# Performance work log

Measured on AMD Instinct MI355X. Metric: run time of the kernel, lower is better.

Reference implementation:

```python
import jax, jax.numpy as jnp
import numpy as np

B, IN, C, M = 256, 512, 4, 6
S1, S2 = 255, 63          # neurons per layer excluding the prepended bias unit
K = 2 ** M                # contexts per neuron
P = 1e-3                  # pred_clipping
LMIN = float(np.log(P / (1.0 - P)))
LMAX = -LMIN
LR = 1e-3                 # constant learning rate
WCLIP = 5.0               # weight_clipping
BASE_BIAS = 0.0           # fixed base bias logit (original draws uniform in [LMIN, LMAX])


def setup_inputs() -> dict:
    key = jax.random.key(0)
    ks = jax.random.split(key, 10)
    x = jax.random.uniform(ks[0], (B, IN), dtype=jnp.float32)
    target = jax.random.randint(ks[1], (B,), 0, C, dtype=jnp.int32)
    cmaps1 = jax.random.normal(ks[2], (C, S1, M, IN), dtype=jnp.float32)
    w1 = jax.random.uniform(ks[3], (C, S1, K, IN), dtype=jnp.float32) * (2.0 / IN)
    bias1 = jax.random.uniform(ks[4], (1, 1, C), dtype=jnp.float32, minval=LMIN, maxval=LMAX)
    cmaps2 = jax.random.normal(ks[5], (C, S2, M, IN), dtype=jnp.float32)
    w2 = jax.random.uniform(ks[6], (C, S2, K, S1 + 1), dtype=jnp.float32) * (2.0 / (S1 + 1))
    bias2 = jax.random.uniform(ks[7], (1, 1, C), dtype=jnp.float32, minval=LMIN, maxval=LMAX)
    cmaps3 = jax.random.normal(ks[8], (C, 1, M, IN), dtype=jnp.float32)
    w3 = jax.random.uniform(ks[9], (C, 1, K, S2 + 1), dtype=jnp.float32) * (2.0 / (S2 + 1))
    return {"x": x, "target": target, "cmaps1": cmaps1, "w1": w1, "bias1": bias1,
            "cmaps2": cmaps2, "w2": w2, "bias2": bias2, "cmaps3": cmaps3, "w3": w3}


def _layer(logit3, context, tgt, cmaps, weights, bias):
    # logit3: (B, I, Cin) with Cin in {1, C}; context: (B, IN); tgt: (B, C) one-hot
    # cmaps: (C, S, M, IN); weights: (C, S, K, I)
    Cn, S = weights.shape[0], weights.shape[1]
    Bn = context.shape[0]
    # context halfspace gating -> per-(class, neuron, sample) context index
    dist = jnp.einsum('csmk,bk->csmb', cmaps, context)          # (C,S,M,B)
    conv = (2 ** jnp.arange(M, dtype=jnp.int32)).reshape(1, 1, M, 1)
    idx = jnp.sum((dist > 0.0).astype(jnp.int32) * conv, axis=2)  # (C,S,B)
    ci = jnp.arange(Cn)[:, None, None]
    si = jnp.arange(S)[None, :, None]
    sel = weights[ci, si, idx]                                  # gather: (C,S,B,I)
    lg = jnp.broadcast_to(logit3, (Bn, logit3.shape[1], Cn))    # (B,I,C)
    out = jnp.clip(jnp.einsum('csbi,bic->csb', sel, lg), LMIN, LMAX)
    out_t = jnp.transpose(out, (2, 1, 0))                       # (B,S,C)
    # online gradient-style update scattered back into the weight table
    diff = jax.nn.sigmoid(out_t) - tgt[:, None, :]              # (B,S,C)
    upd = LR * diff[..., None] * jnp.transpose(lg, (0, 2, 1))[:, None, :, :]  # (B,S,C,I)
    new_w = weights.at[ci, si, idx].set(
        jnp.clip(sel - jnp.transpose(upd, (2, 1, 0, 3)), -WCLIP, WCLIP))
    if bias is not None:
        out_t = jnp.concatenate([jnp.broadcast_to(bias, (Bn, 1, Cn)), out_t], axis=1)
    return out_t, new_w


def reference(x, target, cmaps1, w1, bias1, cmaps2, w2, bias2, cmaps3, w3):
    tgt = jax.nn.one_hot(target, C, dtype=x.dtype)              # (B,C)
    xb = jnp.clip(x, P, 1.0 - P)
    l0 = jnp.log(xb / (1.0 - xb)).at[:, 0].set(BASE_BIAS)       # base predictions in logit space
    out1, nw1 = _layer(l0[:, :, None], x, tgt, cmaps1, w1, bias1)  # (B,256,C)
    out2, nw2 = _layer(out1, x, tgt, cmaps2, w2, bias2)            # (B,64,C)
    out3, nw3 = _layer(out2, x, tgt, cmaps3, w3, None)             # (B,1,C)
    logits = out3[:, 0, :]                                         # (B,C)
    return (logits, nw1, nw2, nw3)
```

## Files before the change

### kernel.cpp

```cpp
#include <hip/hip_runtime.h>
#include <math.h>

#define B_   256
#define IN_  512
#define C_   4
#define M_   6
#define K_   64
#define S1_  255
#define S2_  63

#define NBLK1 (C_ * S1_)
#define NBLK2 (C_ * S2_)
#define NBLK3 (C_)
#define NBLK_ALL (NBLK1 + NBLK2 + NBLK3)

#define LMIN_ (-6.906754778648554f)
#define LMAX_ ( 6.906754778648554f)
#define LR_   0.001f
#define WCLIP_ 5.0f

typedef float v4f __attribute__((ext_vector_type(4)));

__device__ __forceinline__ float clampf(float v, float lo, float hi) {
    return fminf(fmaxf(v, lo), hi);
}

__global__ __launch_bounds__(256) void prep_kernel(const float* __restrict__ x,
                                                   const float* __restrict__ bias1,
                                                   const float* __restrict__ bias2,
                                                   float* __restrict__ xT,
                                                   float* __restrict__ l0,
                                                   float* __restrict__ l0T,
                                                   float* __restrict__ out1T,
                                                   float* __restrict__ out1RM,
                                                   float* __restrict__ out2T,
                                                   float* __restrict__ out2RM) {
    __shared__ float tx_[32][33];
    __shared__ float tl_[32][33];
    const int i0 = (blockIdx.x & 15) * 32;
    const int b0 = (blockIdx.x >> 4) * 32;
    const int tx = threadIdx.x & 31;
    const int ty = threadIdx.x >> 5;
#pragma unroll
    for (int r = 0; r < 4; ++r) {
        int bb = b0 + ty + 8 * r;
        int ii = i0 + tx;
        float xv = x[(size_t)bb * IN_ + ii];
        float xc = clampf(xv, 0.001f, 0.999f);
        float lv = (ii == 0) ? 0.0f : logf(xc / (1.0f - xc));
        l0[(size_t)bb * IN_ + ii] = lv;
        tx_[ty + 8 * r][tx] = xv;
        tl_[ty + 8 * r][tx] = lv;
    }
    __syncthreads();
#pragma unroll
    for (int r = 0; r < 4; ++r) {
        int ii = i0 + ty + 8 * r;
        int bb = b0 + tx;
        xT[(size_t)ii * B_ + bb]  = tx_[tx][ty + 8 * r];
        l0T[(size_t)ii * B_ + bb] = tl_[tx][ty + 8 * r];
    }
    int gid = blockIdx.x * 256 + threadIdx.x;
    if (gid < C_ * B_) {
        int c = gid >> 8, b = gid & 255;
        float b1 = bias1[c], b2 = bias2[c];
        out1T[((size_t)c * (S1_ + 1)) * B_ + b] = b1;
        out1RM[((size_t)c * B_ + b) * (S1_ + 1)] = b1;
        out2T[((size_t)c * (S2_ + 1)) * B_ + b] = b2;
        out2RM[((size_t)c * B_ + b) * (S2_ + 1)] = b2;
    }
}

__global__ __launch_bounds__(256) void route_kernel(
    const float* __restrict__ xT,
    const float* __restrict__ cmaps1,
    const float* __restrict__ cmaps2,
    const float* __restrict__ cmaps3,
    int* __restrict__ idx_buf)
{
    __shared__ float sacc[3][2][M_][B_];
    const int wv   = __builtin_amdgcn_readfirstlane(threadIdx.x >> 6);
    const int lane = threadIdx.x & 63;
    const int t0   = blockIdx.x * 2;

    const float* cmp[2];
#pragma unroll
    for (int u = 0; u < 2; ++u) {
        int bid = t0 + u;
        if (bid < NBLK1)              cmp[u] = cmaps1 + (size_t)bid * M_ * IN_;
        else if (bid < NBLK1 + NBLK2) cmp[u] = cmaps2 + (size_t)(bid - NBLK1) * M_ * IN_;
        else                          cmp[u] = cmaps3 + (size_t)(bid - NBLK1 - NBLK2) * M_ * IN_;
    }

    float acc[2][4][M_];
#pragma unroll
    for (int u = 0; u < 2; ++u)
#pragma unroll
        for (int jb = 0; jb < 4; ++jb)
#pragma unroll
            for (int m = 0; m < M_; ++m) acc[u][jb][m] = 0.0f;

    const int kw = wv * 128;
    for (int k0 = kw; k0 < kw + 128; k0 += 8) {
        float xv[8][4];
#pragma unroll
        for (int j = 0; j < 8; ++j)
#pragma unroll
            for (int jb = 0; jb < 4; ++jb)
                xv[j][jb] = xT[(size_t)(k0 + j) * B_ + 64 * jb + lane];
#pragma unroll
        for (int j = 0; j < 8; ++j)
#pragma unroll
            for (int u = 0; u < 2; ++u)
#pragma unroll
                for (int m = 0; m < M_; ++m) {
                    float cv = cmp[u][(size_t)m * IN_ + k0 + j];
#pragma unroll
                    for (int jb = 0; jb < 4; ++jb)
                        acc[u][jb][m] = fmaf(cv, xv[j][jb], acc[u][jb][m]);
                }
    }

    if (wv > 0) {
#pragma unroll
        for (int u = 0; u < 2; ++u)
#pragma unroll
            for (int jb = 0; jb < 4; ++jb)
#pragma unroll
                for (int m = 0; m < M_; ++m)
                    sacc[wv - 1][u][m][64 * jb + lane] = acc[u][jb][m];
    }
    __syncthreads();
    if (wv == 0) {
#pragma unroll
        for (int u = 0; u < 2; ++u)
#pragma unroll
            for (int jb = 0; jb < 4; ++jb) {
                int b = 64 * jb + lane;
                int myidx = 0;
#pragma unroll
                for (int m = 0; m < M_; ++m) {
                    float t = acc[u][jb][m] + sacc[0][u][m][b] + sacc[1][u][m][b] + sacc[2][u][m][b];
                    myidx |= (t > 0.0f) ? (1 << m) : 0;
                }
                idx_buf[(size_t)(t0 + u) * B_ + b] = myidx;
            }
    }
}

template<int DIN>
__device__ __forceinline__ void dotfin_body(
    int tile,
    const float* __restrict__ lgT, long lgT_sc,
    const float* __restrict__ w,
    const int* __restrict__ idx_buf,
    const int* __restrict__ target,
    float* __restrict__ onextT,
    float* __restrict__ onextRM,
    int* __restrict__ win_g,
    float* __restrict__ dw_g,
    int S,
    float* wl, float* part_s, float* diff_s, int* win_s)
{
    constexpr int HALF = DIN / 2;
    constexpr int NR   = HALF / 64;
    const int c   = tile / S;
    const int s   = tile - c * S;
    const int tid = threadIdx.x;
    const int kh  = __builtin_amdgcn_readfirstlane(tid >> 8);
    const int b   = tid & 255;

    if (tid < K_) win_s[tid] = -1;
    const int myrow = idx_buf[(size_t)tile * B_ + b];

    const float* wp  = w + (size_t)tile * K_ * DIN + kh * HALF;
    float*       dst = wl + kh * (K_ * 65);

    int rrow[4], rq[4];
    float4 pre[4];
#pragma unroll
    for (int j = 0; j < 4; ++j) {
        int f   = b + 256 * j;
        rrow[j] = f >> 4;
        rq[j]   = (f & 15) << 2;
        pre[j]  = *(const float4*)(wp + (size_t)rrow[j] * DIN + rq[j]);
    }

    float dot = 0.0f;
#pragma unroll
    for (int r = 0; r < NR; ++r) {
#pragma unroll
        for (int j = 0; j < 4; ++j) {
            dst[rrow[j] * 65 + rq[j] + 0] = pre[j].x;
            dst[rrow[j] * 65 + rq[j] + 1] = pre[j].y;
            dst[rrow[j] * 65 + rq[j] + 2] = pre[j].z;
            dst[rrow[j] * 65 + rq[j] + 3] = pre[j].w;
        }
        if (r + 1 < NR) {
            const float* src = wp + (r + 1) * 64;
#pragma unroll
            for (int j = 0; j < 4; ++j)
                pre[j] = *(const float4*)(src + (size_t)rrow[j] * DIN + rq[j]);
        }
        __syncthreads();
        const float* lgp = lgT + (size_t)c * lgT_sc + (size_t)(kh * HALF + r * 64) * B_ + b;
        const float* wr  = dst + myrow * 65;
        for (int kk = 0; kk < 64; kk += 8) {
            float lv[8];
#pragma unroll
            for (int t = 0; t < 8; ++t) lv[t] = lgp[(size_t)(kk + t) * B_];
#pragma unroll
            for (int t = 0; t < 8; ++t) dot = fmaf(wr[kk + t], lv[t], dot);
        }
        __syncthreads();
    }
    if (kh == 1) part_s[b] = dot;
    __syncthreads();
    if (kh == 0) {
        float total = dot + part_s[b];
        float outv = clampf(total, LMIN_, LMAX_);
        onextT[((size_t)c * (S + 1) + (s + 1)) * B_ + b] = outv;
        onextRM[((size_t)c * B_ + b) * (size_t)(S + 1) + (s + 1)] = outv;
        float tg = (target[b] == c) ? 1.0f : 0.0f;
        diff_s[b] = 1.0f / (1.0f + expf(-outv)) - tg;
        atomicMax(&win_s[myrow], b);
    }
    __syncthreads();
    if (tid < K_) {
        int bw = win_s[tid];
        win_g[(size_t)tile * K_ + tid] = bw;
        dw_g[(size_t)tile * K_ + tid]  = (bw >= 0) ? LR_ * diff_s[bw] : 0.0f;
    }
}

template<int DIN>
__device__ __forceinline__ void update_body(
    int ub,
    const float* __restrict__ w,
    const float* __restrict__ lgRM, long lg_sc,
    const int* __restrict__ win_g,
    const float* __restrict__ dw_g,
    float* __restrict__ nw,
    int SK)
{
    constexpr int QPR = DIN / 4;
    constexpr int QSH = (DIN == 512) ? 7 : 6;
    const int base = ub * 2048 + threadIdx.x;
    int row[4], col[4], bw[4];
    float d[4];
    float4 wv[4], lv[4];
#pragma unroll
    for (int j = 0; j < 4; ++j) {
        int Q  = base + j * 512;
        row[j] = Q >> QSH;
        col[j] = (Q & (QPR - 1)) << 2;
        wv[j]  = *(const float4*)(w + (size_t)row[j] * DIN + col[j]);
    }
#pragma unroll
    for (int j = 0; j < 4; ++j) {
        bw[j] = win_g[row[j]];
        d[j]  = dw_g[row[j]];
    }
#pragma unroll
    for (int j = 0; j < 4; ++j) {
        int safe = bw[j] < 0 ? 0 : bw[j];
        int cc   = row[j] / SK;
        lv[j] = *(const float4*)(lgRM + (size_t)cc * lg_sc + (size_t)safe * DIN + col[j]);
    }
#pragma unroll
    for (int j = 0; j < 4; ++j) {
        if (bw[j] >= 0) {
            wv[j].x = clampf(wv[j].x - d[j] * lv[j].x, -WCLIP_, WCLIP_);
            wv[j].y = clampf(wv[j].y - d[j] * lv[j].y, -WCLIP_, WCLIP_);
            wv[j].z = clampf(wv[j].z - d[j] * lv[j].z, -WCLIP_, WCLIP_);
            wv[j].w = clampf(wv[j].w - d[j] * lv[j].w, -WCLIP_, WCLIP_);
        }
        v4f o = {wv[j].x, wv[j].y, wv[j].z, wv[j].w};
        __builtin_nontemporal_store(o, (v4f*)(nw + (size_t)row[j] * DIN + col[j]));
    }
}

__global__ __launch_bounds__(512) void dotfin1_kernel(
    const float* __restrict__ l0T,
    const float* __restrict__ w1,
    const int* __restrict__ idx1,
    const int* __restrict__ target,
    float* __restrict__ out1T, float* __restrict__ out1RM,
    int* __restrict__ win1, float* __restrict__ dw1)
{
    __shared__ float wl[2 * K_ * 65];
    __shared__ float part_s[B_];
    __shared__ float diff_s[B_];
    __shared__ int   win_s[K_];
    dotfin_body<512>(blockIdx.x, l0T, 0L, w1, idx1, target,
                     out1T, out1RM, win1, dw1, S1_, wl, part_s, diff_s, win_s);
}

__global__ __launch_bounds__(512) void mix2_kernel(
    const float* __restrict__ out1T,
    const float* __restrict__ w2,
    const int* __restrict__ idx2,
    const int* __restrict__ target,
    float* __restrict__ out2T, float* __restrict__ out2RM,
    int* __restrict__ win2, float* __restrict__ dw2,
    const float* __restrict__ w1,
    const float* __restrict__ l0,
    const int* __restrict__ win1, const float* __restrict__ dw1,
    float* __restrict__ nw1)
{
    __shared__ float wl[2 * K_ * 65];
    __shared__ float part_s[B_];
    __shared__ float diff_s[B_];
    __shared__ int   win_s[K_];
    if ((int)blockIdx.x < NBLK2)
        dotfin_body<256>(blockIdx.x, out1T, (long)(S1_ + 1) * B_, w2, idx2, target,
                         out2T, out2RM, win2, dw2, S2_,
                         wl, part_s, diff_s, win_s);
    else
        update_body<512>(blockIdx.x - NBLK2, w1, l0, 0L, win1, dw1, nw1, S1_ * K_);
}

__device__ __forceinline__ void dotfinup3_body(
    int c,
    const float* __restrict__ lgT, long lgT_sc,
    const float* __restrict__ lgRM, long lg_sc,
    const float* __restrict__ w3,
    const int* __restrict__ idx3,
    const int* __restrict__ target,
    float* __restrict__ nw3,
    float* __restrict__ logits,
    float* wl , float* part_s, float* diff_s, float* dw_s, int* win_s)
{
    const int tid = threadIdx.x;
    const int kh  = __builtin_amdgcn_readfirstlane(tid >> 8);
    const int b   = tid & 255;
    if (tid < K_) win_s[tid] = -1;
    const int myrow = idx3[(size_t)c * B_ + b];

    const float* wp  = w3 + (size_t)c * K_ * 64 + kh * 32;
    float*       dst = wl + kh * (K_ * 33);
#pragma unroll
    for (int j = 0; j < 2; ++j) {
        int f   = b + 256 * j;
        int row = f >> 3;
        int q   = (f & 7) << 2;
        float4 v = *(const float4*)(wp + (size_t)row * 64 + q);
        dst[row * 33 + q + 0] = v.x;
        dst[row * 33 + q + 1] = v.y;
        dst[row * 33 + q + 2] = v.z;
        dst[row * 33 + q + 3] = v.w;
    }
    __syncthreads();
    const float* lgp = lgT + (size_t)c * lgT_sc + (size_t)(kh * 32) * B_ + b;
    const float* wr  = dst + myrow * 33;
    float dot = 0.0f;
    for (int kk = 0; kk < 32; kk += 8) {
        float lv[8];
#pragma unroll
        for (int t = 0; t < 8; ++t) lv[t] = lgp[(size_t)(kk + t) * B_];
#pragma unroll
        for (int t = 0; t < 8; ++t) dot = fmaf(wr[kk + t], lv[t], dot);
    }
    if (kh == 1) part_s[b] = dot;
    __syncthreads();
    if (kh == 0) {
        float total = dot + part_s[b];
        float outv = clampf(total, LMIN_, LMAX_);
        logits[(size_t)b * C_ + c] = outv;
        float tg = (target[b] == c) ? 1.0f : 0.0f;
        diff_s[b] = 1.0f / (1.0f + expf(-outv)) - tg;
        atomicMax(&win_s[myrow], b);
    }
    __syncthreads();
    if (tid < K_) dw_s[tid] = (win_s[tid] >= 0) ? LR_ * diff_s[win_s[tid]] : 0.0f;
    __syncthreads();

    const float* lgc = lgRM + (size_t)c * lg_sc;
    float* nwp = nw3 + (size_t)c * K_ * 64;
#pragma unroll
    for (int j = 0; j < 2; ++j) {
        int Q   = tid + 512 * j;
        int row = Q >> 4;
        int col = (Q & 15) << 2;
        const float* wsrc = wl + (col >> 5) * (K_ * 33) + row * 33 + (col & 31);
        float4 wv = {wsrc[0], wsrc[1], wsrc[2], wsrc[3]};
        int bw = win_s[row];
        if (bw >= 0) {
            float d = dw_s[row];
            const float4 lv = *(const float4*)(lgc + (size_t)bw * 64 + col);
            wv.x = clampf(wv.x - d * lv.x, -WCLIP_, WCLIP_);
            wv.y = clampf(wv.y - d * lv.y, -WCLIP_, WCLIP_);
            wv.z = clampf(wv.z - d * lv.z, -WCLIP_, WCLIP_);
            wv.w = clampf(wv.w - d * lv.w, -WCLIP_, WCLIP_);
        }
        v4f o = {wv.x, wv.y, wv.z, wv.w};
        __builtin_nontemporal_store(o, (v4f*)(nwp + (size_t)row * 64 + col));
    }
}

__global__ __launch_bounds__(512) void mix3_kernel(
    const float* __restrict__ out2T,
    const float* __restrict__ out2RM,
    const float* __restrict__ w3,
    const int* __restrict__ idx3,
    const int* __restrict__ target,
    float* __restrict__ nw3,
    float* __restrict__ logits,
    const float* __restrict__ w2,
    const float* __restrict__ out1RM,
    const int* __restrict__ win2, const float* __restrict__ dw2,
    float* __restrict__ nw2)
{
    __shared__ float wl[2 * K_ * 33];
    __shared__ float part_s[B_];
    __shared__ float diff_s[B_];
    __shared__ float dw_s[K_];
    __shared__ int   win_s[K_];
    if ((int)blockIdx.x < NBLK3)
        dotfinup3_body(blockIdx.x, out2T, (long)(S2_ + 1) * B_,
                       out2RM, (long)B_ * (S2_ + 1), w3, idx3, target,
                       nw3, logits, wl, part_s, diff_s, dw_s, win_s);
    else
        update_body<256>(blockIdx.x - NBLK3, w2, out1RM, (long)B_ * (S1_ + 1),
                         win2, dw2, nw2, S2_ * K_);
}

extern "C" void kernel_launch(void* const* d_in, const int* in_sizes, int n_in,
                              void* d_out, int out_size, void* d_ws, size_t ws_size,
                              hipStream_t stream) {
    const float* x      = (const float*)d_in[0];
    const int*   target = (const int*)  d_in[1];
    const float* cmaps1 = (const float*)d_in[2];
    const float* w1     = (const float*)d_in[3];
    const float* bias1  = (const float*)d_in[4];
    const float* cmaps2 = (const float*)d_in[5];
    const float* w2     = (const float*)d_in[6];
    const float* bias2  = (const float*)d_in[7];
    const float* cmaps3 = (const float*)d_in[8];
    const float* w3     = (const float*)d_in[9];
    float* out = (float*)d_out;

    float* xT      = (float*)d_ws;
    float* l0      = xT     + (size_t)IN_ * B_;
    float* l0T     = l0     + (size_t)B_ * IN_;
    float* out1T   = l0T    + (size_t)IN_ * B_;
    float* out1RM  = out1T  + (size_t)C_ * (S1_ + 1) * B_;
    float* out2T   = out1RM + (size_t)C_ * B_ * (S1_ + 1);
    float* out2RM  = out2T  + (size_t)C_ * (S2_ + 1) * B_;
    float* dw_g    = out2RM + (size_t)C_ * B_ * (S2_ + 1);
    int*   win_g   = (int*)(dw_g + (size_t)(NBLK1 + NBLK2) * K_);
    int*   idx_buf = (int*)(win_g + (size_t)(NBLK1 + NBLK2) * K_);

    float* logits = out;
    float* nw1 = out + (size_t)B_ * C_;
    float* nw2 = nw1 + (size_t)C_ * S1_ * K_ * IN_;
    float* nw3 = nw2 + (size_t)C_ * S2_ * K_ * (S1_ + 1);

    int*   win1 = win_g;                float* dw1 = dw_g;
    int*   win2 = win_g + NBLK1 * K_;   float* dw2 = dw_g + NBLK1 * K_;
    const int* idx1 = idx_buf;
    const int* idx2 = idx_buf + (size_t)NBLK1 * B_;
    const int* idx3 = idx_buf + (size_t)(NBLK1 + NBLK2) * B_;

    prep_kernel<<<dim3(128), dim3(256), 0, stream>>>(
        x, bias1, bias2, xT, l0, l0T, out1T, out1RM, out2T, out2RM);

    route_kernel<<<dim3(NBLK_ALL / 2), dim3(256), 0, stream>>>(
        xT, cmaps1, cmaps2, cmaps3, idx_buf);

    dotfin1_kernel<<<dim3(NBLK1), dim3(512), 0, stream>>>(
        l0T, w1, idx1, target, out1T, out1RM, win1, dw1);

    mix2_kernel<<<dim3(NBLK2 + NBLK1 * 4), dim3(512), 0, stream>>>(
        out1T, w2, idx2, target, out2T, out2RM, win2, dw2,
        w1, l0, win1, dw1, nw1);

    mix3_kernel<<<dim3(NBLK3 + NBLK2 * 2), dim3(512), 0, stream>>>(
        out2T, out2RM, w3, idx3, target, nw3, logits,
        w2, out1RM, win2, dw2, nw2);
}
```

Baseline: 125.3 us.

## Prefetch weight tables during routing and split layer-1 update across kernels

Extra blocks are appended to the routing kernel. They stream through all three weight tables with dummy reads so the data lands in the last-level cache before the gather and update kernels need it. The layer-1 weight-copy/update blocks are also split, half in mix2 and half in mix3, to balance load between the two launches. This adds a full extra read pass over roughly 150MB of weights and relies on the cache being large enough to keep them resident.

Result: slower. 131.4 us (+4.9%).

```diff
diff --git a/kernel.cpp b/kernel.cpp
--- a/kernel.cpp
+++ b/kernel.cpp
@@ -13,6 +13,11 @@
 #define NBLK2 (C_ * S2_)
 #define NBLK3 (C_)
 #define NBLK_ALL (NBLK1 + NBLK2 + NBLK3)
+
+#define NPF   1020
+#define UPB1  4080
+#define UPB1H (UPB1 / 2)
+#define UPB2  504
 
 #define LMIN_ (-6.906754778648554f)
 #define LMAX_ ( 6.906754778648554f)
@@ -71,14 +76,35 @@
     }
 }
 
-__global__ __launch_bounds__(256) void route_kernel(
+__global__ __launch_bounds__(256) void route_pf_kernel(
     const float* __restrict__ xT,
     const float* __restrict__ cmaps1,
     const float* __restrict__ cmaps2,
     const float* __restrict__ cmaps3,
-    int* __restrict__ idx_buf)
+    int* __restrict__ idx_buf,
+    const float* __restrict__ w1,
+    const float* __restrict__ w2,
+    const float* __restrict__ w3)
 {
     __shared__ float sacc[3][2][M_][B_];
+    if ((int)blockIdx.x >= NBLK_ALL / 2) {
+        const int pb = blockIdx.x - NBLK_ALL / 2;
+        const int t  = pb * 256 + threadIdx.x;
+        const int stride = NPF * 256;
+        const int n1 = C_ * S1_ * K_ * IN_ / 4;
+        const int n2 = C_ * S2_ * K_ * (S1_ + 1) / 4;
+        const int n3 = C_ * 1 * K_ * (S2_ + 1) / 4;
+        const float4* w1v = (const float4*)w1;
+        const float4* w2v = (const float4*)w2;
+        const float4* w3v = (const float4*)w3;
+        float s = 0.0f;
+        for (int i = t; i < n1; i += stride) { float4 v = w1v[i]; s += v.x + v.y + v.z + v.w; }
+        for (int i = t; i < n2; i += stride) { float4 v = w2v[i]; s += v.x + v.y + v.z + v.w; }
+        for (int i = t; i < n3; i += stride) { float4 v = w3v[i]; s += v.x + v.y + v.z + v.w; }
+        asm volatile("" :: "v"(s));
+        return;
+    }
+
     const int wv   = __builtin_amdgcn_readfirstlane(threadIdx.x >> 6);
     const int lane = threadIdx.x & 63;
     const int t0   = blockIdx.x * 2;
@@ -329,7 +355,7 @@
     const int* __restrict__ target,
     float* __restrict__ nw3,
     float* __restrict__ logits,
-    float* wl , float* part_s, float* diff_s, float* dw_s, int* win_s)
+    float* wl, float* part_s, float* diff_s, float* dw_s, int* win_s)
 {
     const int tid = threadIdx.x;
     const int kh  = __builtin_amdgcn_readfirstlane(tid >> 8);
@@ -409,7 +435,11 @@
     const float* __restrict__ w2,
     const float* __restrict__ out1RM,
     const int* __restrict__ win2, const float* __restrict__ dw2,
-    float* __restrict__ nw2)
+    float* __restrict__ nw2,
+    const float* __restrict__ w1,
+    const float* __restrict__ l0,
+    const int* __restrict__ win1, const float* __restrict__ dw1,
+    float* __restrict__ nw1)
 {
     __shared__ float wl[2 * K_ * 33];
     __shared__ float part_s[B_];
@@ -420,9 +450,12 @@
         dotfinup3_body(blockIdx.x, out2T, (long)(S2_ + 1) * B_,
                        out2RM, (long)B_ * (S2_ + 1), w3, idx3, target,
                        nw3, logits, wl, part_s, diff_s, dw_s, win_s);
-    else
+    else if ((int)blockIdx.x < NBLK3 + UPB2)
         update_body<256>(blockIdx.x - NBLK3, w2, out1RM, (long)B_ * (S1_ + 1),
                          win2, dw2, nw2, S2_ * K_);
+    else
+        update_body<512>(blockIdx.x - (NBLK3 + UPB2) + UPB1H, w1, l0, 0L,
+                         win1, dw1, nw1, S1_ * K_);
 }
 
 extern "C" void kernel_launch(void* const* d_in, const int* in_sizes, int n_in,
@@ -465,17 +498,18 @@
     prep_kernel<<<dim3(128), dim3(256), 0, stream>>>(
         x, bias1, bias2, xT, l0, l0T, out1T, out1RM, out2T, out2RM);
 
-    route_kernel<<<dim3(NBLK_ALL / 2), dim3(256), 0, stream>>>(
-        xT, cmaps1, cmaps2, cmaps3, idx_buf);
+    route_pf_kernel<<<dim3(NBLK_ALL / 2 + NPF), dim3(256), 0, stream>>>(
+        xT, cmaps1, cmaps2, cmaps3, idx_buf, w1, w2, w3);
 
     dotfin1_kernel<<<dim3(NBLK1), dim3(512), 0, stream>>>(
         l0T, w1, idx1, target, out1T, out1RM, win1, dw1);
 
-    mix2_kernel<<<dim3(NBLK2 + NBLK1 * 4), dim3(512), 0, stream>>>(
+    mix2_kernel<<<dim3(NBLK2 + UPB1H), dim3(512), 0, stream>>>(
         out1T, w2, idx2, target, out2T, out2RM, win2, dw2,
         w1, l0, win1, dw1, nw1);
 
-    mix3_kernel<<<dim3(NBLK3 + NBLK2 * 2), dim3(512), 0, stream>>>(
+    mix3_kernel<<<dim3(NBLK3 + UPB2 + UPB1H), dim3(512), 0, stream>>>(
         out2T, out2RM, w3, idx3, target, nw3, logits,
-        w2, out1RM, win2, dw2, nw2);
-}
+        w2, out1RM, win2, dw2, nw2,
+        w1, l0, win1, dw1, nw1);
+}
```
